# Kernel optimization log

Hardware: AMD Instinct MI355X
Metric: run time of the kernel (lower is better)

## Reference

```python
import jax, jax.numpy as jnp
import numpy as np

NCLASS = 8
THRESH = 0.02
POOL_KS = (32, 16, 8)  # ceil(0.5*64), ceil(0.5*32), ceil(0.5*16)
BN_EPS = 1e-5


def _gcn(x, m, W, b):
    A = m + jnp.eye(x.shape[1], dtype=x.dtype)
    dinv = jax.lax.rsqrt(A.sum(-1))
    An = dinv[:, :, None] * A * dinv[:, None, :]
    return jnp.einsum('bij,bjf->bif', An, x @ W) + b


def _sagpool(x, m, w1, w2, b, k):
    # SAGPooling with GraphConv scorer: s = x w1 + (A x) w2 + b; top-k, gate by tanh
    s = (x @ w1 + jnp.einsum('bij,bjf->bif', m, x) @ w2 + b)[..., 0]
    v, idx = jax.lax.top_k(s, k)
    xg = jnp.take_along_axis(x, idx[:, :, None], axis=1) * jnp.tanh(v)[:, :, None]
    mg = jnp.take_along_axis(jnp.take_along_axis(m, idx[:, :, None], 1), idx[:, None, :], 2)
    return xg, mg


def _readout(x):
    return jnp.concatenate([x.max(1), x.mean(1)], axis=-1)  # [gmp || gep]


def _edist(a, b):
    d2 = (a * a).sum(-1)[:, None] + (b * b).sum(-1)[None, :] - 2.0 * (a @ b.T)
    return jnp.sqrt(jnp.clip(d2, 1e-12))


def _conv1d(x, W, b, dil, pad):
    y = jax.lax.conv_general_dilated(x, W, (1,), [(pad, pad)], rhs_dilation=(dil,),
                                     dimension_numbers=('NCH', 'OIH', 'NCH'))
    return jax.nn.relu(y + b[None, :, None])


def _forward(x, labels, idx_train, gat_W, gat_a1, gat_a2, gcn1_W, gcn1_b, gcn2_W, gcn2_b,
             gcn3_W, gcn3_b, pool1_w1, pool1_w2, pool1_b, pool2_w1, pool2_w2, pool2_b,
             pool3_w1, pool3_w2, pool3_b, gru_Wih, gru_Whh, gru_bih, gru_bhh,
             conv1_W, conv1_b, conv2_W, conv2_b, conv3_W, conv3_b,
             fc0_W, fc0_b, bn0_g, bn0_b, fc1_W, fc1_b, att_W1, att_b1, att_W2, att_b2):
    B, C, L = x.shape
    # GAT-style learned adjacency over the C channel-nodes, thresholded to a sparse graph
    h = x @ gat_W
    e = jax.nn.leaky_relu((h @ gat_a1)[:, :, None] + (h @ gat_a2)[:, None, :], 0.2)
    A = jax.nn.softmax(e, axis=-1)
    m = (A > THRESH).astype(x.dtype)  # [B,C,C] block-diagonal-equivalent mask
    # three GCN + SAGPool stages with summed jump-knowledge readout
    g = jax.nn.relu(_gcn(x, m, gcn1_W, gcn1_b))
    g, m = _sagpool(g, m, pool1_w1, pool1_w2, pool1_b, POOL_KS[0])
    r = _readout(g)
    g = jax.nn.relu(_gcn(g, m, gcn2_W, gcn2_b))
    g, m = _sagpool(g, m, pool2_w1, pool2_w2, pool2_b, POOL_KS[1])
    r = r + _readout(g)
    g = jax.nn.relu(_gcn(g, m, gcn3_W, gcn3_b))
    g, m = _sagpool(g, m, pool3_w1, pool3_w2, pool3_b, POOL_KS[2])
    x_gnn = r + _readout(g)  # [B, 2*hidden]
    # GRU: torch nn.GRU(len_ts, gru_dim) with [N,C,L] -> seq axis 0, batch axis 1 (as in source)
    G = gru_Whh.shape[1]
    def step(hprev, xt):
        gi = xt @ gru_Wih.T + gru_bih
        gh = hprev @ gru_Whh.T + gru_bhh
        ir, iz, inn = jnp.split(gi, 3, axis=-1)
        hr, hz, hn = jnp.split(gh, 3, axis=-1)
        rg = jax.nn.sigmoid(ir + hr)
        zg = jax.nn.sigmoid(iz + hz)
        ng = jnp.tanh(inn + rg * hn)
        hnew = (1.0 - zg) * ng + zg * hprev
        return hnew, hnew
    _, ys = jax.lax.scan(step, jnp.zeros((C, G), x.dtype), x)
    x_gru = ys.mean(1)  # [B, G]
    # dilated conv branch; padding = dilation*(kernel-1) both sides as in __init__
    xc = _conv1d(x, conv1_W, conv1_b, 1, 7)
    xc = _conv1d(xc, conv2_W, conv2_b, 2, 8)
    xc = _conv1d(xc, conv3_W, conv3_b, 4, 8)
    x_conv = xc.mean(2)  # [B, filters[2]]
    feat = jnp.concatenate([x_conv, x_gru, x_gnn], axis=1)
    # mapping MLP: Linear -> BatchNorm(train stats) -> LeakyReLU -> Linear
    hm = feat @ fc0_W + fc0_b
    hm = bn0_g * (hm - hm.mean(0)) * jax.lax.rsqrt(hm.var(0) + BN_EPS) + bn0_b
    hm = jax.nn.leaky_relu(hm, 0.01)
    z = hm @ fc1_W + fc1_b  # [B, 128]
    # per-class attention-weighted prototypes over training samples (masked softmax)
    train = jnp.zeros((B,), bool).at[idx_train].set(True)
    cmask = train[None, :] & (labels[None, :] == jnp.arange(NCLASS)[:, None])
    t = jnp.tanh(jnp.einsum('nd,cda->cna', z, att_W1) + att_b1[:, None, :])
    logits = jnp.einsum('cna,ca->cn', t, att_W2) + att_b2[:, None]
    w = jax.nn.softmax(jnp.where(cmask, logits, -1e30), axis=1)
    proto = w @ z  # [NCLASS, 128]
    pd = jnp.exp(-0.5 * _edist(proto, proto))
    proto_dist = pd.sum() / (NCLASS * (NCLASS - 1) / 2)
    dists = jnp.exp(-0.5 * _edist(z, proto))
    return dists, proto_dist


def setup_inputs() -> dict:
    key = jax.random.key(0)
    ks = iter(jax.random.split(key, 64))
    def rn(shape, s=0.05):
        return jax.random.normal(next(ks), shape, jnp.float32) * s
    B, C, L, H, G, NC, AT, F1 = 256, 64, 512, 128, 128, 8, 64, 128
    inp = {}
    inp['x'] = jax.random.normal(next(ks), (B, C, L), jnp.float32)
    inp['labels'] = jnp.arange(B, dtype=jnp.int32) % NC  # guarantees every class in train split
    inp['idx_train'] = jnp.arange(B // 2, dtype=jnp.int32)
    inp['gat_W'] = rn((L, L)); inp['gat_a1'] = rn((L,)); inp['gat_a2'] = rn((L,))
    inp['gcn1_W'] = rn((L, H)); inp['gcn1_b'] = jnp.zeros((H,), jnp.float32)
    inp['gcn2_W'] = rn((H, H)); inp['gcn2_b'] = jnp.zeros((H,), jnp.float32)
    inp['gcn3_W'] = rn((H, H)); inp['gcn3_b'] = jnp.zeros((H,), jnp.float32)
    for i in (1, 2, 3):
        inp['pool%d_w1' % i] = rn((H, 1)); inp['pool%d_w2' % i] = rn((H, 1))
        inp['pool%d_b' % i] = jnp.zeros((1,), jnp.float32)
    inp['gru_Wih'] = rn((3 * G, L)); inp['gru_Whh'] = rn((3 * G, G))
    inp['gru_bih'] = jnp.zeros((3 * G,), jnp.float32); inp['gru_bhh'] = jnp.zeros((3 * G,), jnp.float32)
    inp['conv1_W'] = rn((F1, C, 8)); inp['conv1_b'] = jnp.zeros((F1,), jnp.float32)
    inp['conv2_W'] = rn((F1, F1, 5)); inp['conv2_b'] = jnp.zeros((F1,), jnp.float32)
    inp['conv3_W'] = rn((F1, F1, 3)); inp['conv3_b'] = jnp.zeros((F1,), jnp.float32)
    inp['fc0_W'] = rn((F1 + G + 2 * H, 256)); inp['fc0_b'] = jnp.zeros((256,), jnp.float32)
    inp['bn0_g'] = jnp.ones((256,), jnp.float32); inp['bn0_b'] = jnp.zeros((256,), jnp.float32)
    inp['fc1_W'] = rn((256, 128)); inp['fc1_b'] = jnp.zeros((128,), jnp.float32)
    inp['att_W1'] = rn((NC, 128, AT)); inp['att_b1'] = jnp.zeros((NC, AT), jnp.float32)
    inp['att_W2'] = rn((NC, AT)); inp['att_b2'] = jnp.zeros((NC,), jnp.float32)
    return inp


def reference(x, labels, idx_train, gat_W, gat_a1, gat_a2, gcn1_W, gcn1_b, gcn2_W, gcn2_b,
              gcn3_W, gcn3_b, pool1_w1, pool1_w2, pool1_b, pool2_w1, pool2_w2, pool2_b,
              pool3_w1, pool3_w2, pool3_b, gru_Wih, gru_Whh, gru_bih, gru_bhh,
              conv1_W, conv1_b, conv2_W, conv2_b, conv3_W, conv3_b,
              fc0_W, fc0_b, bn0_g, bn0_b, fc1_W, fc1_b, att_W1, att_b1, att_W2, att_b2):
    return _forward(x, labels, idx_train, gat_W, gat_a1, gat_a2, gcn1_W, gcn1_b, gcn2_W, gcn2_b,
                    gcn3_W, gcn3_b, pool1_w1, pool1_w2, pool1_b, pool2_w1, pool2_w2, pool2_b,
                    pool3_w1, pool3_w2, pool3_b, gru_Wih, gru_Whh, gru_bih, gru_bhh,
                    conv1_W, conv1_b, conv2_W, conv2_b, conv3_W, conv3_b,
                    fc0_W, fc0_b, bn0_g, bn0_b, fc1_W, fc1_b, att_W1, att_b1, att_W2, att_b2)
```

## Files before the change

### kernel.cpp

```cpp
#include <hip/hip_runtime.h>
#include <math.h>

#define BB 256
#define CC 64
#define LL 512
#define HH 128
#define G3 384
#define NC 8
#define AT 64
#define CL1 519
#define CL2 527
#define CL3 535
#define THRESH 0.02f

typedef _Float16 h2 __attribute__((ext_vector_type(2)));
typedef _Float16 f16x8 __attribute__((ext_vector_type(8)));
typedef float f32x4 __attribute__((ext_vector_type(4)));
union HU { unsigned int u; h2 h; float f; };
union BU { uint4 u; f16x8 h; };

__device__ inline float warp_red_sum(float v) {
  #pragma unroll
  for (int o = 32; o > 0; o >>= 1) v += __shfl_down(v, o, 64);
  return v;
}
__device__ inline float warp_allred_max(float v) {
  #pragma unroll
  for (int o = 32; o > 0; o >>= 1) v = fmaxf(v, __shfl_xor(v, o, 64));
  return v;
}
__device__ inline float warp_allred_sum(float v) {
  #pragma unroll
  for (int o = 32; o > 0; o >>= 1) v += __shfl_xor(v, o, 64);
  return v;
}

__device__ inline float fdot2f(h2 a, h2 b, float c) {
#if __has_builtin(__builtin_amdgcn_fdot2)
  return __builtin_amdgcn_fdot2(a, b, c, false);
#else
  float r;
  asm volatile("v_dot2_f32_f16 %0, %1, %2, %3" : "=v"(r) : "v"(a), "v"(b), "v"(c));
  return r;
#endif
}
__device__ inline h2 asH2(float f) { HU u; u.f = f; return u.h; }
__device__ inline h2 uH2(unsigned int x) { HU u; u.u = x; return u.h; }
__device__ inline unsigned int packh(float a, float b) {
  HU u; h2 t; t.x = (_Float16)a; t.y = (_Float16)b; u.h = t; return u.u;
}
__device__ inline float vexp2(float x) { float r; asm("v_exp_f32 %0, %1" : "=v"(r) : "v"(x)); return r; }
__device__ inline float vrcp(float x)  { float r; asm("v_rcp_f32 %0, %1" : "=v"(r) : "v"(x)); return r; }
__device__ inline float fsigm(float x) { return vrcp(1.f + vexp2(-1.44269504f * x)); }
__device__ inline float ftanh(float x) { return 1.f - 2.f * vrcp(vexp2(2.88539008f * x) + 1.f); }

__global__ void k_wa(const float* __restrict__ gatW, const float* __restrict__ a1,
                     const float* __restrict__ a2, float* wa1, float* wa2) {
  int l = blockIdx.x * 64 + threadIdx.x;
  const float* row = gatW + l * LL;
  float s1 = 0.f, s2 = 0.f;
  for (int k = 0; k < LL; k++) { float w = row[k]; s1 += w * a1[k]; s2 += w * a2[k]; }
  wa1[l] = s1; wa2[l] = s2;
}

__global__ void k_ha(const float* __restrict__ x, const float* __restrict__ wa1,
                     const float* __restrict__ wa2, float* ha1, float* ha2) {
  int wid = threadIdx.x >> 6, lane = threadIdx.x & 63;
  int row = blockIdx.x * 4 + wid;
  const float* xr = x + (size_t)row * LL;
  float s1 = 0.f, s2 = 0.f;
  for (int q = lane; q < LL; q += 64) { float v = xr[q]; s1 += v * wa1[q]; s2 += v * wa2[q]; }
  s1 = warp_red_sum(s1); s2 = warp_red_sum(s2);
  if (lane == 0) { ha1[row] = s1; ha2[row] = s2; }
}

__global__ void k_softmask(const float* __restrict__ ha1, const float* __restrict__ ha2,
                           float* __restrict__ mask, float* __restrict__ dinv) {
  int wid = threadIdx.x >> 6, lane = threadIdx.x & 63;
  int row = blockIdx.x * 4 + wid;
  int b = row >> 6;
  float e = ha1[row] + ha2[b * 64 + lane];
  e = e < 0.f ? 0.2f * e : e;
  float mx = warp_allred_max(e);
  float ex = expf(e - mx);
  float sm = warp_allred_sum(ex);
  float A = ex / sm;
  float mval = (A > THRESH) ? 1.0f : 0.0f;
  mask[(size_t)row * 64 + lane] = mval;
  float cnt = warp_allred_sum(mval);
  if (lane == 0) dinv[row] = 1.0f / sqrtf(cnt + 1.0f);
}

__global__ void k_packall(const float* __restrict__ gcnW0, const float* __restrict__ gcnW1,
                          const float* __restrict__ gcnW2, const float* __restrict__ wih,
                          const float* __restrict__ whh,
                          unsigned int* gw1h, unsigned int* gw2h, unsigned int* gw3h,
                          unsigned int* wihTh, unsigned int* wpk) {
  int idx = blockIdx.x * 256 + threadIdx.x;
  if (idx < 32768) {
    int w_ = idx & 3, l = (idx >> 2) & 63, n = (idx >> 8) & 7, c = idx >> 11;
    int k0 = c * 32 + ((l >> 4) << 3) + 2 * w_;
    int col = n * 16 + (l & 15);
    gw1h[idx] = packh(gcnW0[k0 * 128 + col], gcnW0[(k0 + 1) * 128 + col]);
  } else if (idx < 40960) {
    int t = idx - 32768;
    int w_ = t & 3, l = (t >> 2) & 63, n = (t >> 8) & 7, c = t >> 11;
    int k0 = c * 32 + ((l >> 4) << 3) + 2 * w_;
    int col = n * 16 + (l & 15);
    gw2h[t] = packh(gcnW1[k0 * 128 + col], gcnW1[(k0 + 1) * 128 + col]);
  } else if (idx < 49152) {
    int t = idx - 40960;
    int w_ = t & 3, l = (t >> 2) & 63, n = (t >> 8) & 7, c = t >> 11;
    int k0 = c * 32 + ((l >> 4) << 3) + 2 * w_;
    int col = n * 16 + (l & 15);
    gw3h[t] = packh(gcnW2[k0 * 128 + col], gcnW2[(k0 + 1) * 128 + col]);
  } else if (idx < 147456) {
    int t = idx - 49152;
    int w_ = t & 3, l = (t >> 2) & 63;
    int nfc = t >> 8;
    int n = nfc % 24, c = nfc / 24;
    int k0 = c * 32 + ((l >> 4) << 3) + 2 * w_;
    int col = n * 16 + (l & 15);
    wihTh[t] = packh(wih[col * 512 + k0], wih[col * 512 + k0 + 1]);
  } else if (idx < 172032) {
    int t = idx - 147456; int j = t & 127, rk = t >> 7;
    int r = rk >> 6, k2 = rk & 63;
    const float* src = whh + (size_t)(j + 128 * r) * 128 + 2 * k2;
    wpk[t] = packh(src[0], src[1]);
  }
}

__device__ inline void packw_one(const float* __restrict__ W, unsigned int* __restrict__ out,
                                 int idx, int cinlog, int KS) {
  int w_ = idx & 3, l = (idx >> 2) & 63, n = (idx >> 8) & 7, c = idx >> 11;
  int CIN = 1 << cinlog;
  int oc = n * 16 + (l & 15);
  int k0 = c * 32 + ((l >> 4) << 3) + 2 * w_;
  int t0 = k0 >> cinlog, ci0 = k0 & (CIN - 1);
  int t1 = (k0 + 1) >> cinlog, ci1 = (k0 + 1) & (CIN - 1);
  out[idx] = packh(W[(size_t)oc * CIN * KS + ci0 * KS + t0],
                   W[(size_t)oc * CIN * KS + ci1 * KS + t1]);
}
__global__ void k_packw_mfma(const float* __restrict__ c1W, const float* __restrict__ c2W,
                             const float* __restrict__ c3W, unsigned int* o1,
                             unsigned int* o2, unsigned int* o3) {
  int idx = blockIdx.x * 256 + threadIdx.x;
  if (idx < 32768) packw_one(c1W, o1, idx, 6, 8);
  else if (idx < 73728) packw_one(c2W, o2, idx - 32768, 7, 5);
  else if (idx < 98304) packw_one(c3W, o3, idx - 73728, 7, 3);
}

__global__ __launch_bounds__(256) void k_gmfma(const float* __restrict__ A,
                                               const uint4* __restrict__ Bf,
                                               float* __restrict__ C,
                                               int M, int N, int K) {
  __shared__ _Float16 as[2][64 * 64];
  int nwg = gridDim.x, bid = blockIdx.x;
  int lb = (bid & 7) * (nwg >> 3) + (bid >> 3);
  int nbn = N >> 7;
  int bm = lb / nbn, bn = lb - bm * nbn;
  int m0 = bm * 64;
  int tid = threadIdx.x, l = tid & 63, w = tid >> 6;
  int NKT = K >> 6, NC2 = K >> 5, N16 = N >> 4;
  int nf0 = bn * 8 + 2 * w, nf1 = nf0 + 1;
  int ar = tid >> 2;
  int ac = (tid & 3) * 16;
  float4 rg[4];
  auto stageA = [&](int kt) {
    const float* src = &A[(size_t)(m0 + ar) * K + kt * 64 + ac];
    rg[0] = *(const float4*)&src[0];
    rg[1] = *(const float4*)&src[4];
    rg[2] = *(const float4*)&src[8];
    rg[3] = *(const float4*)&src[12];
  };
  auto commitA = [&](int buf) {
    int s0 = (tid & 3) * 2;
    int phys0 = (s0 ^ (ar & 7)) * 8;
    int phys1 = ((s0 + 1) ^ (ar & 7)) * 8;
    uint4 v0, v1;
    v0.x = packh(rg[0].x, rg[0].y); v0.y = packh(rg[0].z, rg[0].w);
    v0.z = packh(rg[1].x, rg[1].y); v0.w = packh(rg[1].z, rg[1].w);
    v1.x = packh(rg[2].x, rg[2].y); v1.y = packh(rg[2].z, rg[2].w);
    v1.z = packh(rg[3].x, rg[3].y); v1.w = packh(rg[3].z, rg[3].w);
    *(uint4*)&as[buf][ar * 64 + phys0] = v0;
    *(uint4*)&as[buf][ar * 64 + phys1] = v1;
  };
  f32x4 acc[4][2];
  #pragma unroll
  for (int m = 0; m < 4; m++) {
    acc[m][0] = (f32x4){0.f, 0.f, 0.f, 0.f};
    acc[m][1] = (f32x4){0.f, 0.f, 0.f, 0.f};
  }
  stageA(0); commitA(0);
  uint4 bc0 = Bf[(size_t)nf0 * 64 + l];
  uint4 bc1 = Bf[(size_t)nf1 * 64 + l];
  __syncthreads();
  for (int c = 0; c < NC2; c++) {
    int kt = c >> 1, half = c & 1;
    if (half == 0 && kt + 1 < NKT) stageA(kt + 1);
    uint4 pn0 = bc0, pn1 = bc1;
    if (c + 1 < NC2) {
      pn0 = Bf[(size_t)((c + 1) * N16 + nf0) * 64 + l];
      pn1 = Bf[(size_t)((c + 1) * N16 + nf1) * 64 + l];
    }
    int slotbase = half * 4 + (l >> 4);
    f16x8 a[4];
    #pragma unroll
    for (int m = 0; m < 4; m++) {
      int row = m * 16 + (l & 15);
      int phys = slotbase ^ (row & 7);
      a[m] = *(const f16x8*)&as[kt & 1][row * 64 + phys * 8];
    }
    BU u0, u1; u0.u = bc0; u1.u = bc1;
    #pragma unroll
    for (int m = 0; m < 4; m++) {
      acc[m][0] = __builtin_amdgcn_mfma_f32_16x16x32_f16(a[m], u0.h, acc[m][0], 0, 0, 0);
      acc[m][1] = __builtin_amdgcn_mfma_f32_16x16x32_f16(a[m], u1.h, acc[m][1], 0, 0, 0);
    }
    if (half == 1 && kt + 1 < NKT) {
      commitA((kt + 1) & 1);
      __syncthreads();
    }
    bc0 = pn0; bc1 = pn1;
  }
  #pragma unroll
  for (int n = 0; n < 2; n++) {
    int col = (nf0 + n) * 16 + (l & 15);
    #pragma unroll
    for (int m = 0; m < 4; m++) {
      #pragma unroll
      for (int i = 0; i < 4; i++) {
        C[(size_t)(m0 + m * 16 + (l >> 4) * 4 + i) * N + col] = acc[m][n][i];
      }
    }
  }
}

__global__ void k_gcnagg(const float* __restrict__ xw, const float* __restrict__ mask,
                         const float* __restrict__ dinv, const float* __restrict__ bias,
                         float* __restrict__ gout, int N) {
  __shared__ float mrow[64], dv[64];
  int b = blockIdx.x / N, i = blockIdx.x % N;
  if (threadIdx.x < N) {
    mrow[threadIdx.x] = mask[(size_t)(b * N + i) * N + threadIdx.x];
    dv[threadIdx.x] = dinv[b * N + threadIdx.x];
  }
  __syncthreads();
  int f = threadIdx.x;
  float di = dv[i];
  float acc = di * xw[(size_t)(b * N + i) * HH + f];
  for (int j = 0; j < N; j++) acc += mrow[j] * dv[j] * xw[(size_t)(b * N + j) * HH + f];
  float y = di * acc + bias[f];
  gout[(size_t)(b * N + i) * HH + f] = y > 0.f ? y : 0.f;
}

__global__ __launch_bounds__(256) void k_pool(const float* __restrict__ g,
                                              const float* __restrict__ mask,
                                              const float* __restrict__ w1,
                                              const float* __restrict__ w2,
                                              const float* __restrict__ pb, int N, int kk,
                                              float* gp, float* mnext, float* dnext,
                                              float* __restrict__ r) {
  __shared__ float gs[64 * 129];
  __shared__ float ms[64 * 65];
  __shared__ float d1s[64], d2s[64], sv[64], vals[32], tvs[32];
  __shared__ int idxs[32];
  int b = blockIdx.x, tid = threadIdx.x;
  for (int q = tid; q < N * 128; q += 256) {
    int row = q >> 7, d = q & 127;
    gs[row * 129 + d] = g[(size_t)(b * N + row) * 128 + d];
  }
  for (int q = tid; q < N * N; q += 256) {
    int row = q / N, u = q - row * N;
    ms[row * 65 + u] = mask[(size_t)(b * N + row) * N + u];
  }
  __syncthreads();
  if (tid < N) {
    float a = 0.f, c = 0.f;
    const float* gr = &gs[tid * 129];
    for (int d = 0; d < 128; d++) { float v = gr[d]; a += v * w1[d]; c += v * w2[d]; }
    d1s[tid] = a; d2s[tid] = c;
  }
  __syncthreads();
  if (tid < N) {
    const float* mr = &ms[tid * 65];
    float s = d1s[tid] + pb[0];
    for (int j = 0; j < N; j++) s += mr[j] * d2s[j];
    sv[tid] = s;
  }
  __syncthreads();
  if (tid < 64) {
    float myv = (tid < N) ? sv[tid] : -3.4e38f;
    int alive = (tid < N) ? 1 : 0;
    for (int t = 0; t < kk; t++) {
      float cv = alive ? myv : -3.4e38f;
      int ci = tid;
      #pragma unroll
      for (int o = 32; o > 0; o >>= 1) {
        float ov = __shfl_xor(cv, o, 64);
        int oi = __shfl_xor(ci, o, 64);
        if (ov > cv || (ov == cv && oi < ci)) { cv = ov; ci = oi; }
      }
      if (tid == ci) alive = 0;
      if (tid == 0) { idxs[t] = ci; vals[t] = cv; }
    }
  }
  __syncthreads();
  if (tid < kk) tvs[tid] = tanhf(vals[tid]);
  __syncthreads();
  if (tid < HH) {
    float mx = -3.4e38f, sm = 0.f;
    for (int t = 0; t < kk; t++) {
      float v = gs[idxs[t] * 129 + tid] * tvs[t];
      if (gp) gp[(size_t)(b * kk + t) * HH + tid] = v;
      mx = fmaxf(mx, v); sm += v;
    }
    r[b * 256 + tid] += mx;
    r[b * 256 + 128 + tid] += sm / (float)kk;
  }
  for (int q = tid; q < kk * kk; q += 256) {
    int t = q / kk, u = q - t * kk;
    mnext[(size_t)(b * kk + t) * kk + u] = ms[idxs[t] * 65 + idxs[u]];
  }
  if (dnext && tid < kk) {
    float s = 0.f;
    for (int u = 0; u < kk; u++) s += ms[idxs[tid] * 65 + idxs[u]];
    dnext[b * kk + tid] = 1.0f / sqrtf(s + 1.0f);
  }
}

__global__ __launch_bounds__(256, 1) void k_gru(const float* __restrict__ gi,
                                                const unsigned int* __restrict__ wpk,
                                                const float* __restrict__ bhh,
                                                const float* __restrict__ bih,
                                                float* __restrict__ ys) {
  __shared__ _Float16 hb[2][128];
  int c = blockIdx.x;
  int j = threadIdx.x >> 1, half = threadIdx.x & 1;
  int kb = half * 32;
  h2 w0[32], w1[32], w2[32];
  #pragma unroll
  for (int kk = 0; kk < 32; kk++) { HU u; u.u = wpk[(kb + kk) * 128 + j]; w0[kk] = u.h; }
  #pragma unroll
  for (int kk = 0; kk < 32; kk++) { HU u; u.u = wpk[(64 + kb + kk) * 128 + j]; w1[kk] = u.h; }
  #pragma unroll
  for (int kk = 0; kk < 32; kk++) { HU u; u.u = wpk[(128 + kb + kk) * 128 + j]; w2[kk] = u.h; }
  float bh0 = bhh[j], bh1 = bhh[j + 128], bh2 = bhh[j + 256];
  float bi0 = bih[j], bi1 = bih[j + 128], bi2 = bih[j + 256];
  float hprev = 0.f;
  if (half == 0) hb[0][j] = (_Float16)0.f;
  __syncthreads();
  const float* gbase = gi + (size_t)c * G3 + j;
  float g0 = gbase[0], g1 = gbase[128], g2 = gbase[256];
  int cur = 0;
  for (int b = 0; b < BB; b++) {
    float n0 = 0.f, n1 = 0.f, n2 = 0.f;
    if (b + 1 < BB) {
      const float* gn = gbase + (size_t)(b + 1) * CC * G3;
      n0 = gn[0]; n1 = gn[128]; n2 = gn[256];
    }
    float a0a = 0.f, a0b = 0.f, a1a = 0.f, a1b = 0.f, a2a = 0.f, a2b = 0.f;
    #pragma unroll
    for (int q = 0; q < 8; q++) {
      float4 hv = *(const float4*)&hb[cur][half * 64 + q * 8];
      h2 h0 = asH2(hv.x), h1 = asH2(hv.y), h2v = asH2(hv.z), h3 = asH2(hv.w);
      a0a = fdot2f(w0[q * 4 + 0], h0, a0a); a0b = fdot2f(w0[q * 4 + 1], h1, a0b);
      a0a = fdot2f(w0[q * 4 + 2], h2v, a0a); a0b = fdot2f(w0[q * 4 + 3], h3, a0b);
      a1a = fdot2f(w1[q * 4 + 0], h0, a1a); a1b = fdot2f(w1[q * 4 + 1], h1, a1b);
      a1a = fdot2f(w1[q * 4 + 2], h2v, a1a); a1b = fdot2f(w1[q * 4 + 3], h3, a1b);
      a2a = fdot2f(w2[q * 4 + 0], h0, a2a); a2b = fdot2f(w2[q * 4 + 1], h1, a2b);
      a2a = fdot2f(w2[q * 4 + 2], h2v, a2a); a2b = fdot2f(w2[q * 4 + 3], h3, a2b);
    }
    float A0 = a0a + a0b, A1 = a1a + a1b, A2 = a2a + a2b;
    A0 += __shfl_xor(A0, 1, 64);
    A1 += __shfl_xor(A1, 1, 64);
    A2 += __shfl_xor(A2, 1, 64);
    A0 += bh0; A1 += bh1; A2 += bh2;
    float rg = fsigm(g0 + bi0 + A0);
    float zg = fsigm(g1 + bi1 + A1);
    float ng = ftanh(g2 + bi2 + rg * A2);
    float hn = (1.f - zg) * ng + zg * hprev;
    hprev = hn;
    if (half == 0) {
      ys[(size_t)(b * CC + c) * 128 + j] = hn;
      hb[cur ^ 1][j] = (_Float16)hn;
    }
    asm volatile("s_waitcnt lgkmcnt(0)" ::: "memory");
    __builtin_amdgcn_s_barrier();
    cur ^= 1;
    g0 = n0; g1 = n1; g2 = n2;
  }
}

__global__ void k_grumean(const float* __restrict__ ys, float* __restrict__ xgru) {
  int b = blockIdx.x, u = threadIdx.x;
  float acc = 0.f;
  for (int c = 0; c < CC; c++) acc += ys[(size_t)(b * CC + c) * 128 + u];
  xgru[b * 128 + u] = acc / 64.f;
}

template<int CIN, int KS, int DIL, int PAD, int LIN, int LOUT, int MODE>
__global__ __launch_bounds__(256) void k_cmfma(const void* __restrict__ inv,
                                               const uint4* __restrict__ Bf,
                                               const float* __restrict__ bias,
                                               void* __restrict__ outv, int b0) {
  constexpr int QN = CIN / 32;
  constexpr int NCH = KS * QN;
  constexpr int SLOTS = CIN / 8;
  constexpr int NT = (LOUT + 63) / 64;
  __shared__ _Float16 xs[72 * CIN];
  int nb = blockIdx.x / NT;
  int p0 = (blockIdx.x % NT) * 64;
  int tid = threadIdx.x;
  int l = tid & 63, w = tid >> 6;

  if constexpr (MODE == 0) {
    const float* src = (const float*)inv + (size_t)nb * CIN * LIN;
    for (int q = tid; q < (CIN / 2) * 72; q += 256) {
      int ci2 = q / 72, r = q % 72;
      int ci = 2 * ci2;
      int p = p0 - PAD + r;
      float v0 = 0.f, v1 = 0.f;
      if (p >= 0 && p < LIN) { v0 = src[ci * LIN + p]; v1 = src[(ci + 1) * LIN + p]; }
      int slot = ci >> 3;
      int phys = slot ^ (r & 7);
      *(unsigned int*)&xs[r * CIN + phys * 8 + (ci & 7)] = packh(v0, v1);
    }
  } else {
    const _Float16* src = (const _Float16*)inv + (size_t)nb * LIN * CIN;
    for (int q = tid; q < 72 * SLOTS; q += 256) {
      int r = q / SLOTS, s = q % SLOTS;
      int p = p0 - PAD + r;
      uint4 v = make_uint4(0u, 0u, 0u, 0u);
      if (p >= 0 && p < LIN) v = *(const uint4*)&src[(size_t)p * CIN + s * 8];
      int phys = s ^ (r & 7);
      *(uint4*)&xs[r * CIN + phys * 8] = v;
    }
  }
  __syncthreads();

  int n0 = 2 * w, n1 = n0 + 1;
  f32x4 acc[4][2];
  #pragma unroll
  for (int m = 0; m < 4; m++) {
    acc[m][0] = (f32x4){0.f, 0.f, 0.f, 0.f};
    acc[m][1] = (f32x4){0.f, 0.f, 0.f, 0.f};
  }
  uint4 bc0 = Bf[(size_t)(0 * 8 + n0) * 64 + l];
  uint4 bc1 = Bf[(size_t)(0 * 8 + n1) * 64 + l];
  for (int c = 0; c < NCH; c++) {
    uint4 bn0 = bc0, bn1 = bc1;
// ... 9 lines not shown
      int r = m * 16 + (l & 15) + t * DIL;
      int phys = slotbase ^ (r & 7);
      a[m] = *(const f16x8*)&xs[r * CIN + phys * 8];
    }
    BU u0, u1; u0.u = bc0; u1.u = bc1;
    #pragma unroll
    for (int m = 0; m < 4; m++) {
      acc[m][0] = __builtin_amdgcn_mfma_f32_16x16x32_f16(a[m], u0.h, acc[m][0], 0, 0, 0);
      acc[m][1] = __builtin_amdgcn_mfma_f32_16x16x32_f16(a[m], u1.h, acc[m][1], 0, 0, 0);
    }
    bc0 = bn0; bc1 = bn1;
  }

  if constexpr (MODE == 2) {
    float* xcv = (float*)outv;
    #pragma unroll
    for (int n = 0; n < 2; n++) {
      int oc = (2 * w + n) * 16 + (l & 15);
      float bz = bias[oc];
      float s = 0.f;
      #pragma unroll
      for (int m = 0; m < 4; m++) {
        #pragma unroll
        for (int i = 0; i < 4; i++) {
          int pos = p0 + m * 16 + (l >> 4) * 4 + i;
          if (pos < LOUT) { float y = acc[m][n][i] + bz; s += y > 0.f ? y : 0.f; }
        }
      }
      s += __shfl_xor(s, 16, 64);
      s += __shfl_xor(s, 32, 64);
      if (l < 16) atomicAdd(&xcv[(size_t)(b0 + nb) * 128 + oc], s);
    }
  } else {
    _Float16* outp = (_Float16*)outv + (size_t)nb * LOUT * 128;
    #pragma unroll
    for (int n = 0; n < 2; n++) {
      int oc = (2 * w + n) * 16 + (l & 15);
      float bz = bias[oc];
      #pragma unroll
      for (int m = 0; m < 4; m++) {
        #pragma unroll
        for (int i = 0; i < 4; i++) {
          int pos = p0 + m * 16 + (l >> 4) * 4 + i;
          if (pos < LOUT) {
            float y = acc[m][n][i] + bz;
            outp[(size_t)pos * 128 + oc] = (_Float16)(y > 0.f ? y : 0.f);
          }
        }
      }
    }
  }
}

__global__ void k_fc0(const float* __restrict__ xconv, const float* __restrict__ xgru,
                      const float* __restrict__ r, const float* __restrict__ W,
                      const float* __restrict__ bias, float* __restrict__ hm) {
  __shared__ float feat[512];
  int b = blockIdx.x, t = threadIdx.x;
  if (t < 128) { feat[t] = xconv[b * 128 + t] * (1.f / (float)CL3); feat[128 + t] = xgru[b * 128 + t]; }
  feat[256 + t] = r[b * 256 + t];
  __syncthreads();
  float acc = bias[t];
  for (int k = 0; k < 512; k++) acc += feat[k] * W[k * 256 + t];
  hm[b * 256 + t] = acc;
}

__global__ void k_bn(const float* __restrict__ hm, const float* __restrict__ gamma,
                     const float* __restrict__ beta, float* __restrict__ out) {
  __shared__ float red[256];
  int n = blockIdx.x, t = threadIdx.x;
  float v = hm[t * 256 + n];
  red[t] = v; __syncthreads();
  for (int s = 128; s > 0; s >>= 1) { if (t < s) red[t] += red[t + s]; __syncthreads(); }
  float mean = red[0] / 256.f; __syncthreads();
  float dv = v - mean;
  red[t] = dv * dv; __syncthreads();
  for (int s = 128; s > 0; s >>= 1) { if (t < s) red[t] += red[t + s]; __syncthreads(); }
  float var = red[0] / 256.f;
  float y = gamma[n] * dv * (1.f / sqrtf(var + 1e-5f)) + beta[n];
  out[t * 256 + n] = y < 0.f ? 0.01f * y : y;
}

__global__ void k_fc1(const float* __restrict__ hmn, const float* __restrict__ W,
                      const float* __restrict__ bias, float* __restrict__ z) {
  __shared__ float hs[256];
  int b = blockIdx.x, t = threadIdx.x;
  hs[t] = hmn[b * 256 + t]; hs[128 + t] = hmn[b * 256 + 128 + t];
  __syncthreads();
  float acc = bias[t];
  for (int k = 0; k < 256; k++) acc += hs[k] * W[k * 128 + t];
  z[b * 128 + t] = acc;
}

__global__ __launch_bounds__(256) void k_att1(const float* __restrict__ z,
                                              const float* __restrict__ W1,
                                              const float* __restrict__ b1,
                                              const float* __restrict__ W2,
                                              float* __restrict__ logits) {
  __shared__ float sa[32][64];
  __shared__ float sb[32][64];
  int c = blockIdx.x >> 2;
  int m0 = (blockIdx.x & 3) * 64;
  const float* B = W1 + (size_t)c * 128 * AT;
  int tx = threadIdx.x & 15, ty = threadIdx.x >> 4;
  float acc[4][4];
  #pragma unroll
  for (int i = 0; i < 4; i++)
    #pragma unroll
    for (int j = 0; j < 4; j++) acc[i][j] = 0.f;
  int arow = threadIdx.x >> 2;
  int acol = (threadIdx.x & 3) * 8;
  int brow = threadIdx.x >> 4;
  int bcol = (threadIdx.x & 15) * 4;
  for (int k0 = 0; k0 < 128; k0 += 32) {
    float4 av0 = *(const float4*)&z[(size_t)(m0 + arow) * 128 + k0 + acol];
    float4 av1 = *(const float4*)&z[(size_t)(m0 + arow) * 128 + k0 + acol + 4];
    float4 bv0 = *(const float4*)&B[(size_t)(k0 + brow) * AT + bcol];
    float4 bv1 = *(const float4*)&B[(size_t)(k0 + brow + 16) * AT + bcol];
    __syncthreads();
    sa[acol + 0][arow] = av0.x; sa[acol + 1][arow] = av0.y;
    sa[acol + 2][arow] = av0.z; sa[acol + 3][arow] = av0.w;
    sa[acol + 4][arow] = av1.x; sa[acol + 5][arow] = av1.y;
    sa[acol + 6][arow] = av1.z; sa[acol + 7][arow] = av1.w;
    *(float4*)&sb[brow][bcol] = bv0;
    *(float4*)&sb[brow + 16][bcol] = bv1;
    __syncthreads();
    #pragma unroll
    for (int kk = 0; kk < 32; kk++) {
      float4 a4 = *(const float4*)&sa[kk][ty * 4];
      float4 b4 = *(const float4*)&sb[kk][tx * 4];
      acc[0][0] += a4.x * b4.x; acc[0][1] += a4.x * b4.y; acc[0][2] += a4.x * b4.z; acc[0][3] += a4.x * b4.w;
      acc[1][0] += a4.y * b4.x; acc[1][1] += a4.y * b4.y; acc[1][2] += a4.y * b4.z; acc[1][3] += a4.y * b4.w;
      acc[2][0] += a4.z * b4.x; acc[2][1] += a4.z * b4.y; acc[2][2] += a4.z * b4.z; acc[2][3] += a4.z * b4.w;
      acc[3][0] += a4.w * b4.x; acc[3][1] += a4.w * b4.y; acc[3][2] += a4.w * b4.z; acc[3][3] += a4.w * b4.w;
    }
  }
  const float* b1c = b1 + c * AT;
  const float* w2c = W2 + c * AT;
  float w2v[4], b1v[4];
  #pragma unroll
// ... 53 lines not shown
      e = warp_red_sum(e);
      if (t == 0) dout[2048] = e / 28.f;
    }
    return;
  }
  __shared__ float zs[128], red[128];
  int n = blockIdx.x, t = threadIdx.x;
  zs[t] = z[n * 128 + t];
  red[t] = zs[t] * zs[t]; __syncthreads();
  for (int s = 64; s > 0; s >>= 1) { if (t < s) red[t] += red[t + s]; __syncthreads(); }
  float z2 = red[0];
  if (t < NC) {
    float dot = 0.f, p2 = 0.f;
    const float* pr = protos + t * 128;
    for (int d = 0; d < 128; d++) { float pv = pr[d]; dot += pv * zs[d]; p2 += pv * pv; }
    float d2 = fmaxf(z2 + p2 - 2.f * dot, 1e-12f);
    dout[n * NC + t] = expf(-0.5f * sqrtf(d2));
  }
}

extern "C" void kernel_launch(void* const* d_in, const int* in_sizes, int n_in,
                              void* d_out, int out_size, void* d_ws, size_t ws_size,
                              hipStream_t stream) {
  const float* x = (const float*)d_in[0];
  const int* labels = (const int*)d_in[1];
  const int* idx_train = (const int*)d_in[2];
  const float* gat_W = (const float*)d_in[3];
  const float* gat_a1 = (const float*)d_in[4];
  const float* gat_a2 = (const float*)d_in[5];
  const float* gcnW[3] = {(const float*)d_in[6], (const float*)d_in[8], (const float*)d_in[10]};
  const float* gcnB[3] = {(const float*)d_in[7], (const float*)d_in[9], (const float*)d_in[11]};
  const float* pw1[3] = {(const float*)d_in[12], (const float*)d_in[15], (const float*)d_in[18]};
  const float* pw2[3] = {(const float*)d_in[13], (const float*)d_in[16], (const float*)d_in[19]};
  const float* pbb[3] = {(const float*)d_in[14], (const float*)d_in[17], (const float*)d_in[20]};
  const float* wih = (const float*)d_in[21];
  const float* whh = (const float*)d_in[22];
  const float* bih = (const float*)d_in[23];
  const float* bhh = (const float*)d_in[24];
  const float* c1W = (const float*)d_in[25]; const float* c1b = (const float*)d_in[26];
  const float* c2W = (const float*)d_in[27]; const float* c2b = (const float*)d_in[28];
  const float* c3W = (const float*)d_in[29]; const float* c3b = (const float*)d_in[30];
  const float* fc0W = (const float*)d_in[31]; const float* fc0b = (const float*)d_in[32];
  const float* bn0g = (const float*)d_in[33]; const float* bn0b = (const float*)d_in[34];
  const float* fc1W = (const float*)d_in[35]; const float* fc1b = (const float*)d_in[36];
  const float* aW1 = (const float*)d_in[37]; const float* ab1 = (const float*)d_in[38];
  const float* aW2 = (const float*)d_in[39]; const float* ab2 = (const float*)d_in[40];
  float* out = (float*)d_out;
  float* ws = (float*)d_ws;

  size_t off = 0;
  auto take = [&](size_t n) { size_t o = off; off += (n + 63) & ~(size_t)63; return o; };
  float* wa1   = ws + take(512);
  float* wa2   = ws + take(512);
  float* ha1   = ws + take(BB * CC);
  float* ha2   = ws + take(BB * CC);
  float* dinv  = ws + take(BB * 64);
  float* rbuf  = ws + take(BB * 256);
  float* xgru  = ws + take(BB * 128);
  float* xconv = ws + take(BB * 128);
  float* hm    = ws + take(BB * 256);
  float* hmn   = ws + take(BB * 256);
  float* zb    = ws + take(BB * 128);
  float* protos = ws + take(NC * 128);
  float* lgts  = ws + take(NC * 256);
  float* gw1h  = ws + take(256 * 128);
  float* gw2h  = ws + take(64 * 128);
  float* gw3h  = ws + take(64 * 128);
  float* wpkf  = ws + take(192 * 128);
  float* wslot = ws + take(512 * 384);
  float* Z     = ws + take(8568832);
  float* mA  = Z;
  float* mB  = Z + 1048576;
  float* xw  = Z + 2097152;
  float* gb  = Z + 4194304;
  float* gp1 = Z + 6291456;
  float* gp2 = Z + 7340032;
  float* gi = Z;
  float* ys = Z + 6291456;
  float* cv1 = Z;
  float* cv2 = Z + 4251648;
  unsigned int* wpk = (unsigned int*)wpkf;
  unsigned int* wihTh = (unsigned int*)wslot;
  unsigned int* wt1h = (unsigned int*)wslot;
  unsigned int* wt2h = wt1h + 32768;
  unsigned int* wt3h = wt2h + 40960;

  hipMemsetAsync(rbuf, 0, BB * 256 * sizeof(float), stream);
  hipMemsetAsync(xconv, 0, BB * 128 * sizeof(float), stream);

  k_wa<<<8, 64, 0, stream>>>(gat_W, gat_a1, gat_a2, wa1, wa2);
  k_packall<<<672, 256, 0, stream>>>(gcnW[0], gcnW[1], gcnW[2], wih, whh,
                                     (unsigned int*)gw1h, (unsigned int*)gw2h,
                                     (unsigned int*)gw3h, wihTh, wpk);
  k_ha<<<BB * CC / 4, 256, 0, stream>>>(x, wa1, wa2, ha1, ha2);
  k_softmask<<<BB * 64 / 4, 256, 0, stream>>>(ha1, ha2, mA, dinv);

  const int Ns[3] = {64, 32, 16};
  const int ks[3] = {32, 16, 8};
  const int Kin[3] = {512, 128, 128};
  const float* gins[3] = {x, gp1, gp2};
  const unsigned int* gwh[3] = {(unsigned int*)gw1h, (unsigned int*)gw2h, (unsigned int*)gw3h};
  float* mcur[3] = {mA, mB, mA};
  float* mnxt[3] = {mB, mA, mB};
  float* gps[3]  = {gp1, gp2, nullptr};
  for (int s = 0; s < 3; s++) {
    int N = Ns[s];
    k_gmfma<<<(BB * N / 64), 256, 0, stream>>>(
        gins[s], (const uint4*)gwh[s], xw, BB * N, HH, Kin[s]);
    k_gcnagg<<<BB * N, 128, 0, stream>>>(xw, mcur[s], dinv, gcnB[s], gb, N);
    k_pool<<<BB, 256, 0, stream>>>(gb, mcur[s], pw1[s], pw2[s], pbb[s], N, ks[s],
                                   gps[s], mnxt[s], s < 2 ? dinv : nullptr, rbuf);
  }

  k_gmfma<<<(BB * CC / 64) * 3, 256, 0, stream>>>(
      x, (const uint4*)wihTh, gi, BB * CC, G3, LL);
  k_gru<<<CC, 256, 0, stream>>>(gi, wpk, bhh, bih, ys);
  k_grumean<<<BB, 128, 0, stream>>>(ys, xgru);

  k_packw_mfma<<<384, 256, 0, stream>>>(c1W, c2W, c3W, wt1h, wt2h, wt3h);
  for (int bc = 0; bc < 2; bc++) {
    int b0 = bc * 128;
    k_cmfma<64, 8, 1, 7, 512, CL1, 0><<<128 * 9, 256, 0, stream>>>(
        x + (size_t)b0 * CC * LL, (const uint4*)wt1h, c1b, cv1, b0);
    k_cmfma<128, 5, 2, 8, CL1, CL2, 1><<<128 * 9, 256, 0, stream>>>(
        cv1, (const uint4*)wt2h, c2b, cv2, b0);
    k_cmfma<128, 3, 4, 8, CL2, CL3, 2><<<128 * 9, 256, 0, stream>>>(
        cv2, (const uint4*)wt3h, c3b, xconv, b0);
  }

  k_fc0<<<BB, 256, 0, stream>>>(xconv, xgru, rbuf, fc0W, fc0b, hm);
  k_bn<<<256, 256, 0, stream>>>(hm, bn0g, bn0b, hmn);
  k_fc1<<<BB, 128, 0, stream>>>(hmn, fc1W, fc1b, zb);
  k_att1<<<NC * 4, 256, 0, stream>>>(zb, aW1, ab1, aW2, lgts);
  k_att2<<<NC, 256, 0, stream>>>(zb, labels, idx_train, in_sizes[2], lgts, ab2, protos);
  k_dist<<<BB + 1, 128, 0, stream>>>(zb, protos, out);
}
```

Before: 486.2 us.

## Fuse small launches: merge packing, GAT mask, GRU mean and batchnorm kernels

Folds the conv weight packing and the gat_W·a projections into the single packing kernel. It replaces the k_ha and k_softmask kernels with one per-batch GAT kernel, and lets the pooling stage overwrite the readout buffer on its first pass so that memset goes away. GRU outputs are stored in fp16 and averaged inside fc0, and batchnorm statistics are gathered with atomics in fc0 and applied inside fc1. This cuts kernel launches and intermediate traffic. In exchange it adds atomic contention, a one-pass variance formula with reduced numerical robustness, and fp16 rounding of the GRU outputs.

```diff
diff --git a/kernel.cpp b/kernel.cpp
--- a/kernel.cpp
+++ b/kernel.cpp
@@ -24,16 +24,6 @@
   for (int o = 32; o > 0; o >>= 1) v += __shfl_down(v, o, 64);
   return v;
 }
-__device__ inline float warp_allred_max(float v) {
-  #pragma unroll
-  for (int o = 32; o > 0; o >>= 1) v = fmaxf(v, __shfl_xor(v, o, 64));
-  return v;
-}
-__device__ inline float warp_allred_sum(float v) {
-  #pragma unroll
-  for (int o = 32; o > 0; o >>= 1) v += __shfl_xor(v, o, 64);
-  return v;
-}
 
 __device__ inline float fdot2f(h2 a, h2 b, float c) {
 #if __has_builtin(__builtin_amdgcn_fdot2)
@@ -54,48 +44,29 @@
 __device__ inline float fsigm(float x) { return vrcp(1.f + vexp2(-1.44269504f * x)); }
 __device__ inline float ftanh(float x) { return 1.f - 2.f * vrcp(vexp2(2.88539008f * x) + 1.f); }
 
-__global__ void k_wa(const float* __restrict__ gatW, const float* __restrict__ a1,
-                     const float* __restrict__ a2, float* wa1, float* wa2) {
-  int l = blockIdx.x * 64 + threadIdx.x;
-  const float* row = gatW + l * LL;
-  float s1 = 0.f, s2 = 0.f;
-  for (int k = 0; k < LL; k++) { float w = row[k]; s1 += w * a1[k]; s2 += w * a2[k]; }
-  wa1[l] = s1; wa2[l] = s2;
-}
-
-__global__ void k_ha(const float* __restrict__ x, const float* __restrict__ wa1,
-                     const float* __restrict__ wa2, float* ha1, float* ha2) {
-  int wid = threadIdx.x >> 6, lane = threadIdx.x & 63;
-  int row = blockIdx.x * 4 + wid;
-  const float* xr = x + (size_t)row * LL;
-  float s1 = 0.f, s2 = 0.f;
-  for (int q = lane; q < LL; q += 64) { float v = xr[q]; s1 += v * wa1[q]; s2 += v * wa2[q]; }
-  s1 = warp_red_sum(s1); s2 = warp_red_sum(s2);
-  if (lane == 0) { ha1[row] = s1; ha2[row] = s2; }
-}
-
-__global__ void k_softmask(const float* __restrict__ ha1, const float* __restrict__ ha2,
-                           float* __restrict__ mask, float* __restrict__ dinv) {
-  int wid = threadIdx.x >> 6, lane = threadIdx.x & 63;
-  int row = blockIdx.x * 4 + wid;
-  int b = row >> 6;
-  float e = ha1[row] + ha2[b * 64 + lane];
-  e = e < 0.f ? 0.2f * e : e;
-  float mx = warp_allred_max(e);
-  float ex = expf(e - mx);
-  float sm = warp_allred_sum(ex);
-  float A = ex / sm;
-  float mval = (A > THRESH) ? 1.0f : 0.0f;
-  mask[(size_t)row * 64 + lane] = mval;
-  float cnt = warp_allred_sum(mval);
-  if (lane == 0) dinv[row] = 1.0f / sqrtf(cnt + 1.0f);
+__device__ inline void packw_one(const float* __restrict__ W, unsigned int* __restrict__ out,
+                                 int idx, int cinlog, int KS) {
+  int w_ = idx & 3, l = (idx >> 2) & 63, n = (idx >> 8) & 7, c = idx >> 11;
+  int CIN = 1 << cinlog;
+  int oc = n * 16 + (l & 15);
+  int k0 = c * 32 + ((l >> 4) << 3) + 2 * w_;
+  int t0 = k0 >> cinlog, ci0 = k0 & (CIN - 1);
+  int t1 = (k0 + 1) >> cinlog, ci1 = (k0 + 1) & (CIN - 1);
+  out[idx] = packh(W[(size_t)oc * CIN * KS + ci0 * KS + t0],
+                   W[(size_t)oc * CIN * KS + ci1 * KS + t1]);
 }
 
 __global__ void k_packall(const float* __restrict__ gcnW0, const float* __restrict__ gcnW1,
                           const float* __restrict__ gcnW2, const float* __restrict__ wih,
                           const float* __restrict__ whh,
+                          const float* __restrict__ c1W, const float* __restrict__ c2W,
+                          const float* __restrict__ c3W,
+                          const float* __restrict__ gatW, const float* __restrict__ a1,
+                          const float* __restrict__ a2,
                           unsigned int* gw1h, unsigned int* gw2h, unsigned int* gw3h,
-                          unsigned int* wihTh, unsigned int* wpk) {
+                          unsigned int* wihTh, unsigned int* wpk,
+                          unsigned int* wt1h, unsigned int* wt2h, unsigned int* wt3h,
+                          float* wa1, float* wa2) {
   int idx = blockIdx.x * 256 + threadIdx.x;
   if (idx < 32768) {
     int w_ = idx & 3, l = (idx >> 2) & 63, n = (idx >> 8) & 7, c = idx >> 11;
@@ -127,33 +98,74 @@
     int r = rk >> 6, k2 = rk & 63;
     const float* src = whh + (size_t)(j + 128 * r) * 128 + 2 * k2;
     wpk[t] = packh(src[0], src[1]);
-  }
-}
-
-__device__ inline void packw_one(const float* __restrict__ W, unsigned int* __restrict__ out,
-                                 int idx, int cinlog, int KS) {
-  int w_ = idx & 3, l = (idx >> 2) & 63, n = (idx >> 8) & 7, c = idx >> 11;
-  int CIN = 1 << cinlog;
-  int oc = n * 16 + (l & 15);
-  int k0 = c * 32 + ((l >> 4) << 3) + 2 * w_;
-  int t0 = k0 >> cinlog, ci0 = k0 & (CIN - 1);
-  int t1 = (k0 + 1) >> cinlog, ci1 = (k0 + 1) & (CIN - 1);
-  out[idx] = packh(W[(size_t)oc * CIN * KS + ci0 * KS + t0],
-                   W[(size_t)oc * CIN * KS + ci1 * KS + t1]);
-}
-__global__ void k_packw_mfma(const float* __restrict__ c1W, const float* __restrict__ c2W,
-                             const float* __restrict__ c3W, unsigned int* o1,
-                             unsigned int* o2, unsigned int* o3) {
-  int idx = blockIdx.x * 256 + threadIdx.x;
-  if (idx < 32768) packw_one(c1W, o1, idx, 6, 8);
-  else if (idx < 73728) packw_one(c2W, o2, idx - 32768, 7, 5);
-  else if (idx < 98304) packw_one(c3W, o3, idx - 73728, 7, 3);
+  } else if (idx < 204800) {
+    packw_one(c1W, wt1h, idx - 172032, 6, 8);
+  } else if (idx < 245760) {
+    packw_one(c2W, wt2h, idx - 204800, 7, 5);
+  } else if (idx < 270336) {
+    packw_one(c3W, wt3h, idx - 245760, 7, 3);
+  } else if (idx < 270848) {
+    int l = idx - 270336;
+    const float* row = gatW + l * LL;
+    float s1 = 0.f, s2 = 0.f;
+    for (int k = 0; k < LL; k++) { float w = row[k]; s1 += w * a1[k]; s2 += w * a2[k]; }
+    wa1[l] = s1; wa2[l] = s2;
+  }
+}
+
+__global__ __launch_bounds__(256) void k_gat(const float* __restrict__ x,
+                                             const float* __restrict__ wa1,
+                                             const float* __restrict__ wa2,
+                                             float* __restrict__ mask,
+                                             float* __restrict__ dinv) {
+  __shared__ float h1s[64], h2s[64];
+  int b = blockIdx.x, tid = threadIdx.x;
+  int i = tid >> 2, q = tid & 3;
+  const float* xr = x + ((size_t)b * 64 + i) * LL + q * 128;
+  float s1 = 0.f, s2 = 0.f;
+  #pragma unroll 4
+  for (int k = 0; k < 128; k += 4) {
+    float4 xv = *(const float4*)&xr[k];
+    float4 w1 = *(const float4*)&wa1[q * 128 + k];
+    float4 w2 = *(const float4*)&wa2[q * 128 + k];
+    s1 += xv.x * w1.x + xv.y * w1.y + xv.z * w1.z + xv.w * w1.w;
+    s2 += xv.x * w2.x + xv.y * w2.y + xv.z * w2.z + xv.w * w2.w;
+  }
+  s1 += __shfl_xor(s1, 1, 64); s1 += __shfl_xor(s1, 2, 64);
+  s2 += __shfl_xor(s2, 1, 64); s2 += __shfl_xor(s2, 2, 64);
+  if (q == 0) { h1s[i] = s1; h2s[i] = s2; }
+  __syncthreads();
+  float hi = h1s[i];
+  float e[16];
+  float mx = -3.4e38f;
+  #pragma unroll
+  for (int u = 0; u < 16; u++) {
+    float v = hi + h2s[q * 16 + u];
+    v = v < 0.f ? 0.2f * v : v;
+    e[u] = v;
+    mx = fmaxf(mx, v);
+  }
+  mx = fmaxf(mx, __shfl_xor(mx, 1, 64));
+  mx = fmaxf(mx, __shfl_xor(mx, 2, 64));
+  float sm = 0.f;
+  #pragma unroll
+  for (int u = 0; u < 16; u++) { e[u] = expf(e[u] - mx); sm += e[u]; }
+  sm += __shfl_xor(sm, 1, 64); sm += __shfl_xor(sm, 2, 64);
+  float cnt = 0.f;
+  #pragma unroll
+  for (int u = 0; u < 16; u++) {
+    float mval = (e[u] / sm > THRESH) ? 1.f : 0.f;
+    mask[((size_t)b * 64 + i) * 64 + q * 16 + u] = mval;
+    cnt += mval;
+  }
+  cnt += __shfl_xor(cnt, 1, 64); cnt += __shfl_xor(cnt, 2, 64);
+  if (q == 0) dinv[b * 64 + i] = 1.f / sqrtf(cnt + 1.f);
 }
 
 __global__ __launch_bounds__(256) void k_gmfma(const float* __restrict__ A,
                                                const uint4* __restrict__ Bf,
-                                               float* __restrict__ C,
-                                               int M, int N, int K) {
+                                               void* __restrict__ Cv,
+                                               int M, int N, int K, int out16) {
   __shared__ _Float16 as[2][64 * 64];
   int nwg = gridDim.x, bid = blockIdx.x;
   int lb = (bid & 7) * (nwg >> 3) + (bid >> 3);
@@ -223,14 +235,28 @@
     }
     bc0 = pn0; bc1 = pn1;
   }
-  #pragma unroll
-  for (int n = 0; n < 2; n++) {
-    int col = (nf0 + n) * 16 + (l & 15);
-    #pragma unroll
-    for (int m = 0; m < 4; m++) {
+  if (out16) {
+    _Float16* Ch = (_Float16*)Cv;
+    #pragma unroll
+    for (int n = 0; n < 2; n++) {
+      int col = (nf0 + n) * 16 + (l & 15);
       #pragma unroll
-      for (int i = 0; i < 4; i++) {
-        C[(size_t)(m0 + m * 16 + (l >> 4) * 4 + i) * N + col] = acc[m][n][i];
+      for (int m = 0; m < 4; m++) {
+        #pragma unroll
+        for (int i = 0; i < 4; i++)
+          Ch[(size_t)(m0 + m * 16 + (l >> 4) * 4 + i) * N + col] = (_Float16)acc[m][n][i];
+      }
+    }
+  } else {
+    float* Cf = (float*)Cv;
+    #pragma unroll
+    for (int n = 0; n < 2; n++) {
+      int col = (nf0 + n) * 16 + (l & 15);
+      #pragma unroll
+      for (int m = 0; m < 4; m++) {
+        #pragma unroll
+        for (int i = 0; i < 4; i++)
+          Cf[(size_t)(m0 + m * 16 + (l >> 4) * 4 + i) * N + col] = acc[m][n][i];
       }
     }
   }
@@ -260,7 +286,7 @@
                                               const float* __restrict__ w2,
                                               const float* __restrict__ pb, int N, int kk,
                                               float* gp, float* mnext, float* dnext,
-                                              float* __restrict__ r) {
+                                              float* __restrict__ r, int accum) {
   __shared__ float gs[64 * 129];
   __shared__ float ms[64 * 65];
   __shared__ float d1s[64], d2s[64], sv[64], vals[32], tvs[32];
@@ -315,8 +341,14 @@
       if (gp) gp[(size_t)(b * kk + t) * HH + tid] = v;
       mx = fmaxf(mx, v); sm += v;
     }
-    r[b * 256 + tid] += mx;
-    r[b * 256 + 128 + tid] += sm / (float)kk;
+    float mres = sm / (float)kk;
+    if (accum) {
+      r[b * 256 + tid] += mx;
+      r[b * 256 + 128 + tid] += mres;
+    } else {
+      r[b * 256 + tid] = mx;
+      r[b * 256 + 128 + tid] = mres;
+    }
   }
   for (int q = tid; q < kk * kk; q += 256) {
     int t = q / kk, u = q - t * kk;
@@ -333,7 +365,7 @@
                                                 const unsigned int* __restrict__ wpk,
                                                 const float* __restrict__ bhh,
                                                 const float* __restrict__ bih,
-                                                float* __restrict__ ys) {
+                                                _Float16* __restrict__ ys) {
   __shared__ _Float16 hb[2][128];
   int c = blockIdx.x;
   int j = threadIdx.x >> 1, half = threadIdx.x & 1;
@@ -382,7 +414,7 @@
     float hn = (1.f - zg) * ng + zg * hprev;
     hprev = hn;
     if (half == 0) {
-      ys[(size_t)(b * CC + c) * 128 + j] = hn;
+      ys[(size_t)(b * CC + c) * 128 + j] = (_Float16)hn;
       hb[cur ^ 1][j] = (_Float16)hn;
     }
     asm volatile("s_waitcnt lgkmcnt(0)" ::: "memory");
@@ -390,13 +422,6 @@
     cur ^= 1;
     g0 = n0; g1 = n1; g2 = n2;
   }
-}
-
-__global__ void k_grumean(const float* __restrict__ ys, float* __restrict__ xgru) {
-  int b = blockIdx.x, u = threadIdx.x;
-  float acc = 0.f;
-  for (int c = 0; c < CC; c++) acc += ys[(size_t)(b * CC + c) * 128 + u];
-  xgru[b * 128 + u] = acc / 64.f;
 }
 
 template<int CIN, int KS, int DIL, int PAD, int LIN, int LOUT, int MODE>
@@ -512,40 +537,41 @@
   }
 }
 
-__global__ void k_fc0(const float* __restrict__ xconv, const float* __restrict__ xgru,
+__global__ void k_fc0(const float* __restrict__ xconv, const _Float16* __restrict__ ys,
                       const float* __restrict__ r, const float* __restrict__ W,
-                      const float* __restrict__ bias, float* __restrict__ hm) {
+                      const float* __restrict__ bias, float* __restrict__ hm,
+                      float* __restrict__ csum, float* __restrict__ csum2) {
   __shared__ float feat[512];
   int b = blockIdx.x, t = threadIdx.x;
-  if (t < 128) { feat[t] = xconv[b * 128 + t] * (1.f / (float)CL3); feat[128 + t] = xgru[b * 128 + t]; }
+  if (t < 128) {
+    feat[t] = xconv[b * 128 + t] * (1.f / (float)CL3);
+    const _Float16* yb = ys + (size_t)b * CC * 128 + t;
+    float acc = 0.f;
+    for (int c = 0; c < CC; c++) acc += (float)yb[c * 128];
+    feat[128 + t] = acc / 64.f;
+  }
   feat[256 + t] = r[b * 256 + t];
   __syncthreads();
   float acc = bias[t];
   for (int k = 0; k < 512; k++) acc += feat[k] * W[k * 256 + t];
   hm[b * 256 + t] = acc;
-}
-
-__global__ void k_bn(const float* __restrict__ hm, const float* __restrict__ gamma,
-                     const float* __restrict__ beta, float* __restrict__ out) {
-  __shared__ float red[256];
-  int n = blockIdx.x, t = threadIdx.x;
-  float v = hm[t * 256 + n];
-  red[t] = v; __syncthreads();
-  for (int s = 128; s > 0; s >>= 1) { if (t < s) red[t] += red[t + s]; __syncthreads(); }
-  float mean = red[0] / 256.f; __syncthreads();
-  float dv = v - mean;
-  red[t] = dv * dv; __syncthreads();
-  for (int s = 128; s > 0; s >>= 1) { if (t < s) red[t] += red[t + s]; __syncthreads(); }
-  float var = red[0] / 256.f;
-  float y = gamma[n] * dv * (1.f / sqrtf(var + 1e-5f)) + beta[n];
-  out[t * 256 + n] = y < 0.f ? 0.01f * y : y;
-}
-
-__global__ void k_fc1(const float* __restrict__ hmn, const float* __restrict__ W,
-                      const float* __restrict__ bias, float* __restrict__ z) {
+  atomicAdd(&csum[t], acc);
+  atomicAdd(&csum2[t], acc * acc);
+}
+
+__global__ void k_fc1bn(const float* __restrict__ hm, const float* __restrict__ csum,
+                        const float* __restrict__ csum2, const float* __restrict__ gamma,
+                        const float* __restrict__ beta, const float* __restrict__ W,
+                        const float* __restrict__ bias, float* __restrict__ z) {
   __shared__ float hs[256];
   int b = blockIdx.x, t = threadIdx.x;
-  hs[t] = hmn[b * 256 + t]; hs[128 + t] = hmn[b * 256 + 128 + t];
+  for (int kk = t; kk < 256; kk += 128) {
+    float v = hm[b * 256 + kk];
+    float mean = csum[kk] * (1.f / 256.f);
+    float var = csum2[kk] * (1.f / 256.f) - mean * mean;
+    float y = gamma[kk] * (v - mean) * (1.f / sqrtf(var + 1e-5f)) + beta[kk];
+    hs[kk] = y < 0.f ? 0.01f * y : y;
+  }
   __syncthreads();
   float acc = bias[t];
   for (int k = 0; k < 256; k++) acc += hs[k] * W[k * 128 + t];
@@ -705,22 +731,22 @@
   auto take = [&](size_t n) { size_t o = off; off += (n + 63) & ~(size_t)63; return o; };
   float* wa1   = ws + take(512);
   float* wa2   = ws + take(512);
-  float* ha1   = ws + take(BB * CC);
-  float* ha2   = ws + take(BB * CC);
   float* dinv  = ws + take(BB * 64);
   float* rbuf  = ws + take(BB * 256);
-  float* xgru  = ws + take(BB * 128);
   float* xconv = ws + take(BB * 128);
+  float* csum  = ws + take(256);
+  float* csum2 = ws + take(256);
   float* hm    = ws + take(BB * 256);
-  float* hmn   = ws + take(BB * 256);
   float* zb    = ws + take(BB * 128);
   float* protos = ws + take(NC * 128);
   float* lgts  = ws + take(NC * 256);
+  float* ysf   = ws + take(1048576);
   float* gw1h  = ws + take(256 * 128);
   float* gw2h  = ws + take(64 * 128);
   float* gw3h  = ws + take(64 * 128);
   float* wpkf  = ws + take(192 * 128);
-  float* wslot = ws + take(512 * 384);
+  float* wihThf = ws + take(98304);
+  float* wtcf  = ws + take(98304);
   float* Z     = ws + take(8568832);
   float* mA  = Z;
   float* mB  = Z + 1048576;
@@ -729,24 +755,24 @@
   float* gp1 = Z + 6291456;
   float* gp2 = Z + 7340032;
   float* gi = Z;
-  float* ys = Z + 6291456;
   float* cv1 = Z;
   float* cv2 = Z + 4251648;
+  _Float16* ysh = (_Float16*)ysf;
   unsigned int* wpk = (unsigned int*)wpkf;
-  unsigned int* wihTh = (unsigned int*)wslot;
-  unsigned int* wt1h = (unsigned int*)wslot;
+  unsigned int* wihTh = (unsigned int*)wihThf;
+  unsigned int* wt1h = (unsigned int*)wtcf;
   unsigned int* wt2h = wt1h + 32768;
   unsigned int* wt3h = wt2h + 40960;
 
-  hipMemsetAsync(rbuf, 0, BB * 256 * sizeof(float), stream);
-  hipMemsetAsync(xconv, 0, BB * 128 * sizeof(float), stream);
-
-  k_wa<<<8, 64, 0, stream>>>(gat_W, gat_a1, gat_a2, wa1, wa2);
-  k_packall<<<672, 256, 0, stream>>>(gcnW[0], gcnW[1], gcnW[2], wih, whh,
-                                     (unsigned int*)gw1h, (unsigned int*)gw2h,
-                                     (unsigned int*)gw3h, wihTh, wpk);
-  k_ha<<<BB * CC / 4, 256, 0, stream>>>(x, wa1, wa2, ha1, ha2);
-  k_softmask<<<BB * 64 / 4, 256, 0, stream>>>(ha1, ha2, mA, dinv);
+  hipMemsetAsync(xconv, 0, (BB * 128 + 512) * sizeof(float), stream);
+
+  k_packall<<<1058, 256, 0, stream>>>(gcnW[0], gcnW[1], gcnW[2], wih, whh,
+                                      c1W, c2W, c3W, gat_W, gat_a1, gat_a2,
+                                      (unsigned int*)gw1h, (unsigned int*)gw2h,
+                                      (unsigned int*)gw3h, wihTh, wpk,
+                                      wt1h, wt2h, wt3h, wa1, wa2);
+
+  k_gat<<<BB, 256, 0, stream>>>(x, wa1, wa2, mA, dinv);
 
   const int Ns[3] = {64, 32, 16};
   const int ks[3] = {32, 16, 8};
@@ -759,18 +785,16 @@
   for (int s = 0; s < 3; s++) {
     int N = Ns[s];
     k_gmfma<<<(BB * N / 64), 256, 0, stream>>>(
-        gins[s], (const uint4*)gwh[s], xw, BB * N, HH, Kin[s]);
+        gins[s], (const uint4*)gwh[s], xw, BB * N, HH, Kin[s], 0);
     k_gcnagg<<<BB * N, 128, 0, stream>>>(xw, mcur[s], dinv, gcnB[s], gb, N);
     k_pool<<<BB, 256, 0, stream>>>(gb, mcur[s], pw1[s], pw2[s], pbb[s], N, ks[s],
-                                   gps[s], mnxt[s], s < 2 ? dinv : nullptr, rbuf);
+                                   gps[s], mnxt[s], s < 2 ? dinv : nullptr, rbuf, s);
   }
 
   k_gmfma<<<(BB * CC / 64) * 3, 256, 0, stream>>>(
-      x, (const uint4*)wihTh, gi, BB * CC, G3, LL);
-  k_gru<<<CC, 256, 0, stream>>>(gi, wpk, bhh, bih, ys);
-  k_grumean<<<BB, 128, 0, stream>>>(ys, xgru);
-
-  k_packw_mfma<<<384, 256, 0, stream>>>(c1W, c2W, c3W, wt1h, wt2h, wt3h);
+      x, (const uint4*)wihTh, gi, BB * CC, G3, LL, 0);
+  k_gru<<<CC, 256, 0, stream>>>(gi, wpk, bhh, bih, ysh);
+
   for (int bc = 0; bc < 2; bc++) {
     int b0 = bc * 128;
     k_cmfma<64, 8, 1, 7, 512, CL1, 0><<<128 * 9, 256, 0, stream>>>(
@@ -781,9 +805,8 @@
         cv2, (const uint4*)wt3h, c3b, xconv, b0);
   }
 
-  k_fc0<<<BB, 256, 0, stream>>>(xconv, xgru, rbuf, fc0W, fc0b, hm);
-  k_bn<<<256, 256, 0, stream>>>(hm, bn0g, bn0b, hmn);
-  k_fc1<<<BB, 128, 0, stream>>>(hmn, fc1W, fc1b, zb);
+  k_fc0<<<BB, 256, 0, stream>>>(xconv, ysh, rbuf, fc0W, fc0b, hm, csum, csum2);
+  k_fc1bn<<<BB, 128, 0, stream>>>(hm, csum, csum2, bn0g, bn0b, fc1W, fc1b, zb);
   k_att1<<<NC * 4, 256, 0, stream>>>(zb, aW1, ab1, aW2, lgts);
   k_att2<<<NC, 256, 0, stream>>>(zb, labels, idx_train, in_sizes[2], lgts, ab2, protos);
   k_dist<<<BB + 1, 128, 0, stream>>>(zb, protos, out);
```

New measurement: 484.9 us. About the same (-0.3%).
